# Optimization experiments

Measured on AMD Instinct MI355X. Metric: run time of the kernel, lower is better.

## Reference

```python
import jax, jax.numpy as jnp
import numpy as np

B = 16
H = 56
W = 56
C = 384
NH = 12
HD = C // NH
WS = 7
SHIFT = 3
N = WS * WS
SCALE = HD ** -0.5
EPS = 1e-3  # keras LayerNormalization default epsilon


def _rel_pos_index():
    coords = np.stack(np.meshgrid(np.arange(WS), np.arange(WS), indexing='ij')).reshape(2, -1)
    rel = (coords[:, :, None] - coords[:, None, :]).transpose(1, 2, 0)
    rel[:, :, 0] += WS - 1
    rel[:, :, 1] += WS - 1
    rel[:, :, 0] *= 2 * WS - 1
    return rel.sum(-1)  # [N, N]

REL_IDX = jnp.asarray(_rel_pos_index())


def _shift_mask():
    # faithful reproduction of the TransformerBlock.__init__ mask construction
    mask = np.zeros((1, H, W, 1), np.float32)
    slices = (slice(0, -WS), slice(-WS, -SHIFT), slice(-SHIFT, None))
    cnt = 0
    for hs in slices:
        for ws in slices:
            mask[:, hs, ws, :] = cnt
            cnt += 1
    mw = mask.reshape(1, H // WS, WS, W // WS, WS, 1).transpose(0, 1, 3, 2, 4, 5).reshape(-1, N)
    m = mw[:, None, :] - mw[:, :, None]  # expand_dims(mw,1) - expand_dims(mw,2)
    return np.where(m != 0, np.float32(-100.0), np.float32(0.0))  # [nw, N, N]

MASK = jnp.asarray(_shift_mask())


def _ln(x, g, b):
    mu = x.mean(-1, keepdims=True)
    var = ((x - mu) ** 2).mean(-1, keepdims=True)
    return (x - mu) / jnp.sqrt(var + EPS) * g + b


def _window_partition(x):  # [B,H,W,C] -> [B*nw, N, C]
    b = x.shape[0]
    x = x.reshape(b, H // WS, WS, W // WS, WS, C).transpose(0, 1, 3, 2, 4, 5)
    return x.reshape(-1, N, C)


def _window_reverse(wins, b):  # [B*nw, WS, WS, C] -> [B,H,W,C]
    x = wins.reshape(b, H // WS, W // WS, WS, WS, C).transpose(0, 1, 3, 2, 4, 5)
    return x.reshape(b, H, W, C)


def setup_inputs() -> dict:
    key = jax.random.key(0)
    ks = jax.random.split(key, 8)
    s = 0.02
    return {
        'x': jax.random.normal(ks[0], (B, H * W, C), jnp.float32),
        'ln1_g': jnp.ones((C,), jnp.float32),
        'ln1_b': jnp.zeros((C,), jnp.float32),
        'ln2_g': jnp.ones((C,), jnp.float32),
        'ln2_b': jnp.zeros((C,), jnp.float32),
        'qkv_w': s * jax.random.normal(ks[1], (C, 3 * C), jnp.float32),
        'qkv_b': jnp.zeros((3 * C,), jnp.float32),
        'proj_w': s * jax.random.normal(ks[2], (C, C), jnp.float32),
        'proj_b': jnp.zeros((C,), jnp.float32),
        'mlp_w1': s * jax.random.normal(ks[3], (C, 4 * C), jnp.float32),
        'mlp_b1': jnp.zeros((4 * C,), jnp.float32),
        'mlp_w2': s * jax.random.normal(ks[4], (4 * C, C), jnp.float32),
        'mlp_b2': jnp.zeros((C,), jnp.float32),
        'rel_pos_table': s * jax.random.normal(ks[5], ((2 * WS - 1) * (2 * WS - 1), NH), jnp.float32),
    }


def reference(x, ln1_g, ln1_b, ln2_g, ln2_b, qkv_w, qkv_b, proj_w, proj_b,
              mlp_w1, mlp_b1, mlp_w2, mlp_b2, rel_pos_table):
    skip = x
    y = _ln(x, ln1_g, ln1_b).reshape(B, H, W, C)
    # cyclic shift (faithful to source: shift=(-s, +s))
    y = jnp.roll(y, shift=(-SHIFT, SHIFT), axis=(1, 2))
    wins = _window_partition(y)                      # [nW, N, C]
    nW = wins.shape[0]

    qkv = wins @ qkv_w + qkv_b                       # [nW, N, 3C]
    qkv = qkv.reshape(nW, N, 3, NH, HD).transpose(2, 0, 3, 1, 4)
    q, k, v = qkv[0] * SCALE, qkv[1], qkv[2]         # [nW, NH, N, HD]

    attn = jnp.einsum('whnd,whmd->whnm', q, k)       # [nW, NH, N, N]
    bias = rel_pos_table[REL_IDX.reshape(-1)].reshape(N, N, NH).transpose(2, 0, 1)
    attn = attn + bias[None]

    nw = MASK.shape[0]
    attn = attn.reshape(nW // nw, nw, NH, N, N) + MASK[None, :, None]
    attn = jax.nn.softmax(attn.reshape(nW, NH, N, N), axis=-1)

    out = jnp.einsum('whnm,whmd->wnhd', attn, v).reshape(nW, N, C)
    out = out @ proj_w + proj_b

    y = _window_reverse(out.reshape(-1, WS, WS, C), B)
    # reverse shift (faithful to source: shift=(+s, +s))
    y = jnp.roll(y, shift=(SHIFT, SHIFT), axis=(1, 2))
    x = y.reshape(B, H * W, C) + skip

    skip = x
    y = _ln(x, ln2_g, ln2_b)
    y = jax.nn.gelu(y @ mlp_w1 + mlp_b1, approximate=False)
    y = y @ mlp_w2 + mlp_b2
    return y + skip
```

## Files before the change

### kernel.cpp

```cpp
#include <hip/hip_runtime.h>
#include <hip/hip_bf16.h>
#include <math.h>

typedef __hip_bfloat16 bf16;
typedef unsigned short ushort_t;
typedef __bf16 bf16x8 __attribute__((ext_vector_type(8)));
typedef float f32x4 __attribute__((ext_vector_type(4)));

#define TOKENS 50176
#define CW2 512
#define CROWS2 (CW2 * 49)
#define SCALE_ 0.17677669529663687f

__device__ __forceinline__ float b2f(bf16 v) { return __bfloat162float(v); }
__device__ __forceinline__ bf16  f2b(float v) { return __float2bfloat16(v); }

__device__ __forceinline__ float gelu_f(float v) {
  float x = v * 0.7071067811865475f;
  float ax = fabsf(x);
  float t = 1.f / (1.f + 0.3275911f * ax);
  float poly = ((((1.061405429f * t - 1.453152027f) * t + 1.421413741f) * t
                 - 0.284496736f) * t + 0.254829592f) * t;
  float erfv = 1.f - poly * __expf(-ax * ax);
  erfv = copysignf(erfv, x);
  return 0.5f * v * (1.f + erfv);
}

__global__ __launch_bounds__(256) void wt_bf16(const float* __restrict__ W,
                                               ushort_t* __restrict__ Wt,
                                               int K, int N) {
  int idx = blockIdx.x * 256 + threadIdx.x;
  if (idx >= K * N) return;
  int n = idx / K, k = idx - n * K;
  bf16 h = f2b(W[(size_t)k * N + n]);
  Wt[idx] = *(ushort_t*)&h;
}

__global__ __launch_bounds__(64) void ln1_kernel(const float* __restrict__ x,
                                                 const float* __restrict__ g,
                                                 const float* __restrict__ bta,
                                                 bf16* __restrict__ wins) {
  int t = blockIdx.x;
  int lane = threadIdx.x;
  int w = t / 49, n = t - w * 49;
  int bi = w >> 6, wi = w & 63;
  int hw = wi >> 3, ww = wi & 7;
  int ti = n / 7, tj = n - ti * 7;
  int hr = hw * 7 + ti, wr = ww * 7 + tj;
  int hs = (hr + 3) % 56;
  int wsc = (wr + 53) % 56;
  const float* row = x + ((size_t)bi * 3136 + hs * 56 + wsc) * 384;
  float v[6];
  float s = 0.f, s2 = 0.f;
#pragma unroll
  for (int j = 0; j < 6; ++j) {
    v[j] = row[lane + 64 * j];
    s += v[j]; s2 += v[j] * v[j];
  }
#pragma unroll
  for (int m = 32; m >= 1; m >>= 1) {
    s  += __shfl_xor(s, m, 64);
    s2 += __shfl_xor(s2, m, 64);
  }
  float mu = s * (1.f / 384.f);
  float var = s2 * (1.f / 384.f) - mu * mu;
  float rstd = rsqrtf(var + 1e-3f);
  bf16* orow = wins + (size_t)t * 384;
#pragma unroll
  for (int j = 0; j < 6; ++j) {
    int c = lane + 64 * j;
    orow[c] = f2b((v[j] - mu) * rstd * g[c] + bta[c]);
  }
}

__global__ __launch_bounds__(64) void ln2_kernel(const float* __restrict__ x1,
                                                 const float* __restrict__ g,
                                                 const float* __restrict__ bta,
                                                 bf16* __restrict__ out) {
  int t = blockIdx.x;
  int lane = threadIdx.x;
  const float* row = x1 + (size_t)t * 384;
  float v[6];
  float s = 0.f, s2 = 0.f;
#pragma unroll
  for (int j = 0; j < 6; ++j) {
    v[j] = row[lane + 64 * j];
    s += v[j]; s2 += v[j] * v[j];
  }
#pragma unroll
  for (int m = 32; m >= 1; m >>= 1) {
    s  += __shfl_xor(s, m, 64);
    s2 += __shfl_xor(s2, m, 64);
  }
  float mu = s * (1.f / 384.f);
  float var = s2 * (1.f / 384.f) - mu * mu;
  float rstd = rsqrtf(var + 1e-3f);
  bf16* orow = out + (size_t)t * 384;
#pragma unroll
  for (int j = 0; j < 6; ++j) {
    int c = lane + 64 * j;
    orow[c] = f2b((v[j] - mu) * rstd * g[c] + bta[c]);
  }
}

template<int MODE>
__global__ __launch_bounds__(512, 6) void mfma_gemm(
    const ushort_t* __restrict__ A, const ushort_t* __restrict__ Bt,
    const float* __restrict__ bias, int N, int K,
    const float* __restrict__ resid, void* __restrict__ out_) {
  __shared__ ushort_t As[128 * 32];
  __shared__ ushort_t Bs[128 * 32];
  int tid = threadIdx.x;
  int lane = tid & 63, wv = tid >> 6;
  int wm = wv >> 1, wn = wv & 1;
  int lm = lane & 15, kg = lane >> 4;

  int nwg = gridDim.x;
  int q = nwg >> 3, r = nwg & 7;
  int xcd = blockIdx.x & 7, ii = blockIdx.x >> 3;
  int l = ((xcd < r) ? xcd * (q + 1) : r * (q + 1) + (xcd - r) * q) + ii;
  int nxt = N >> 7;
  int col0 = (l % nxt) * 128, row0 = (l / nxt) * 128;

  f32x4 acc[2][4];
#pragma unroll
  for (int i = 0; i < 2; ++i)
#pragma unroll
    for (int j = 0; j < 4; ++j) acc[i][j] = (f32x4){0.f, 0.f, 0.f, 0.f};

  int rsub = lane >> 2;
  int bsrc = (lane & 3) ^ ((rsub >> 1) & 3);
  int pbr = kg ^ ((lm >> 1) & 3);

  const ushort_t* gA = &A[(size_t)(row0 + wv * 16 + rsub) * K + bsrc * 8];
  const ushort_t* gB = &Bt[(size_t)(col0 + wv * 16 + rsub) * K + bsrc * 8];

  int NT = K >> 5;
  for (int t = 0; t < NT; ++t) {
    __builtin_amdgcn_global_load_lds(
        (const __attribute__((address_space(1))) void*)(gA + (t << 5)),
        (__attribute__((address_space(3))) void*)&As[wv * 512], 16, 0, 0);
    __builtin_amdgcn_global_load_lds(
        (const __attribute__((address_space(1))) void*)(gB + (t << 5)),
        (__attribute__((address_space(3))) void*)&Bs[wv * 512], 16, 0, 0);
    __syncthreads();
    bf16x8 a[2], b[4];
#pragma unroll
    for (int i = 0; i < 2; ++i) {
      int ra = wm * 32 + i * 16 + lm;
      a[i] = *(const bf16x8*)&As[ra * 32 + pbr * 8];
    }
#pragma unroll
    for (int j = 0; j < 4; ++j) {
      int rb = wn * 64 + j * 16 + lm;
      b[j] = *(const bf16x8*)&Bs[rb * 32 + pbr * 8];
    }
#pragma unroll
    for (int i = 0; i < 2; ++i)
#pragma unroll
      for (int j = 0; j < 4; ++j)
        acc[i][j] = __builtin_amdgcn_mfma_f32_16x16x32_bf16(a[i], b[j], acc[i][j], 0, 0, 0);
    __syncthreads();
  }

  int m0 = row0 + wm * 32, n0 = col0 + wn * 64;
#pragma unroll
  for (int i = 0; i < 2; ++i) {
#pragma unroll
    for (int reg = 0; reg < 4; ++reg) {
      int m = m0 + i * 16 + kg * 4 + reg;
      size_t obase = 0;
      if (MODE == 1) {
        int w = m / 49, nn = m - w * 49;
        int bi = w >> 6, wi = w & 63;
        int hw = wi >> 3, ww = wi & 7;
        int ti = nn / 7, tj = nn - ti * 7;
        int hf = (hw * 7 + ti + 3) % 56, wf = (ww * 7 + tj + 3) % 56;
        obase = ((size_t)bi * 3136 + hf * 56 + wf) * 384;
      }
#pragma unroll
      for (int j = 0; j < 4; ++j) {
        int cN = n0 + j * 16 + lm;
        float v = acc[i][j][reg] + bias[cN];
        if (MODE == 0) {
          ((bf16*)out_)[(size_t)m * N + cN] = f2b(v);
        } else if (MODE == 1) {
          float* O = (float*)out_;
          O[obase + cN] = v + resid[obase + cN];
        } else if (MODE == 2) {
          ((bf16*)out_)[(size_t)m * N + cN] = f2b(gelu_f(v));
        } else {
          float* O = (float*)out_;
          O[(size_t)m * N + cN] = v + resid[(size_t)m * N + cN];
        }
      }
    }
  }
}

__global__ __launch_bounds__(256) void attn_mfma(const ushort_t* __restrict__ qkv_c,
                                                 const float* __restrict__ table,
                                                 ushort_t* __restrict__ attn_c,
                                                 int w_base) {
  int wl = blockIdx.x >> 2, hg = blockIdx.x & 3;
  int w = w_base + wl;
  int wi = w & 63;
  int hw = wi >> 3, ww = wi & 7;
  __shared__ ushort_t Qs[64 * 40];
  __shared__ ushort_t Ks[64 * 40];
  __shared__ ushort_t Vt[32 * 72];
  __shared__ ushort_t Ps[64 * 72];
  __shared__ float bias_s[169 * 12];
  int tid = threadIdx.x;
  int lane = tid & 63, wv = tid >> 6;
  int lm = lane & 15, kg = lane >> 4;

  for (int i = tid; i < 64 * 40; i += 256) { Qs[i] = 0; Ks[i] = 0; }
  for (int i = tid; i < 32 * 72; i += 256) Vt[i] = 0;
  for (int i = tid; i < 169 * 12; i += 256) bias_s[i] = table[i];
  __syncthreads();

  for (int hh = 0; hh < 3; ++hh) {
    int h = hg * 3 + hh;
    const ushort_t* base = qkv_c + (size_t)wl * 49 * 1152 + h * 32;
    for (int idx = tid; idx < 392; idx += 256) {
      int n = idx >> 3, d0 = (idx & 7) * 4;
      const ushort_t* p = base + (size_t)n * 1152 + d0;
      ushort4 q = *(const ushort4*)(p);
      ushort4 k = *(const ushort4*)(p + 384);
      ushort4 v = *(const ushort4*)(p + 768);
      *(ushort4*)&Qs[n * 40 + d0] = q;
      *(ushort4*)&Ks[n * 40 + d0] = k;
      Vt[(d0 + 0) * 72 + n] = v.x;
      Vt[(d0 + 1) * 72 + n] = v.y;
      Vt[(d0 + 2) * 72 + n] = v.z;
      Vt[(d0 + 3) * 72 + n] = v.w;
    }
    __syncthreads();

    bf16x8 qa = *(const bf16x8*)&Qs[(wv * 16 + lm) * 40 + kg * 8];
    f32x4 sacc[4];
#pragma unroll
    for (int jt = 0; jt < 4; ++jt) {
      bf16x8 kb = *(const bf16x8*)&Ks[(jt * 16 + lm) * 40 + kg * 8];
      sacc[jt] = __builtin_amdgcn_mfma_f32_16x16x32_bf16(
          qa, kb, (f32x4){0.f, 0.f, 0.f, 0.f}, 0, 0, 0);
    }

    int i_base = wv * 16 + kg * 4;
#pragma unroll
    for (int reg = 0; reg < 4; ++reg) {
      int i = i_base + reg;
      int ii = (i < 49) ? i : 0;
      int yi = ii / 7, xi = ii - yi * 7;
      int hri = hw * 7 + yi, wri = ww * 7 + xi;
      int ri = (hri < 49 ? 0 : (hri < 53 ? 1 : 2)) * 3 + (wri < 49 ? 0 : (wri < 53 ? 1 : 2));
      float sv[4];
      float mx = -1e30f;
#pragma unroll
      for (int jt = 0; jt < 4; ++jt) {
        int j = jt * 16 + lm;
        int jj = (j < 49) ? j : 0;
        int yj = jj / 7, xj = jj - yj * 7;
        int hrj = hw * 7 + yj, wrj = ww * 7 + xj;
        int rj = (hrj < 49 ? 0 : (hrj < 53 ? 1 : 2)) * 3 + (wrj < 49 ? 0 : (wrj < 53 ? 1 : 2));
        int ridx = (yi - yj + 6) * 13 + (xi - xj + 6);
        float s = sacc[jt][reg] * SCALE_ + bias_s[ridx * 12 + h] + ((ri == rj) ? 0.f : -100.f);
        sv[jt] = (j < 49) ? s : -1e30f;
        mx = fmaxf(mx, sv[jt]);
      }
#pragma unroll
      for (int msk = 1; msk < 16; msk <<= 1) mx = fmaxf(mx, __shfl_xor(mx, msk, 64));
      float sm = 0.f;
#pragma unroll
      for (int jt = 0; jt < 4; ++jt) {
        float e = ((jt * 16 + lm) < 49) ? __expf(sv[jt] - mx) : 0.f;
        sv[jt] = e; sm += e;
      }
#pragma unroll
      for (int msk = 1; msk < 16; msk <<= 1) sm += __shfl_xor(sm, msk, 64);
      float inv = 1.f / sm;
#pragma unroll
      for (int jt = 0; jt < 4; ++jt) {
        bf16 pb = f2b(sv[jt] * inv);
        Ps[(size_t)i * 72 + jt * 16 + lm] = *(ushort_t*)&pb;
      }
    }
    f32x4 oacc[2] = {(f32x4){0.f, 0.f, 0.f, 0.f}, (f32x4){0.f, 0.f, 0.f, 0.f}};
#pragma unroll
    for (int ks = 0; ks < 2; ++ks) {
      bf16x8 pa = *(const bf16x8*)&Ps[(wv * 16 + lm) * 72 + ks * 32 + kg * 8];
#pragma unroll
      for (int dt = 0; dt < 2; ++dt) {
        bf16x8 vb = *(const bf16x8*)&Vt[(dt * 16 + lm) * 72 + ks * 32 + kg * 8];
        oacc[dt] = __builtin_amdgcn_mfma_f32_16x16x32_bf16(pa, vb, oacc[dt], 0, 0, 0);
      }
    }
#pragma unroll
    for (int reg = 0; reg < 4; ++reg) {
      int r = i_base + reg;
      if (r < 49) {
#pragma unroll
        for (int dt = 0; dt < 2; ++dt) {
          bf16 ob = f2b(oacc[dt][reg]);
          attn_c[((size_t)wl * 49 + r) * 384 + h * 32 + dt * 16 + lm] = *(ushort_t*)&ob;
        }
      }
    }
    __syncthreads();
  }
}

extern "C" void kernel_launch(void* const* d_in, const int* in_sizes, int n_in,
                              void* d_out, int out_size, void* d_ws, size_t ws_size,
                              hipStream_t stream) {
  const float* x      = (const float*)d_in[0];
  const float* ln1_g  = (const float*)d_in[1];
  const float* ln1_b  = (const float*)d_in[2];
  const float* ln2_g  = (const float*)d_in[3];
  const float* ln2_b  = (const float*)d_in[4];
  const float* qkv_w  = (const float*)d_in[5];
  const float* qkv_b  = (const float*)d_in[6];
  const float* proj_w = (const float*)d_in[7];
  const float* proj_b = (const float*)d_in[8];
  const float* mlp_w1 = (const float*)d_in[9];
  const float* mlp_b1 = (const float*)d_in[10];
  const float* mlp_w2 = (const float*)d_in[11];
  const float* mlp_b2 = (const float*)d_in[12];
  const float* rel_tb = (const float*)d_in[13];

  char* ws = (char*)d_ws;
  ushort_t* r0 = (ushort_t*)(ws + 0);
  ushort_t* r1 = (ushort_t*)(ws + 38535168ull);
  ushort_t* wq = (ushort_t*)(ws + 115605504ull);
  ushort_t* wp = wq + 442368;
  ushort_t* w1 = wp + 147456;
  ushort_t* w2 = w1 + 589824;
  float* out = (float*)d_out;

  wt_bf16<<<1728, 256, 0, stream>>>(qkv_w, wq, 384, 1152);
  wt_bf16<<<576, 256, 0, stream>>>(proj_w, wp, 384, 384);
  wt_bf16<<<2304, 256, 0, stream>>>(mlp_w1, w1, 384, 1536);
  wt_bf16<<<2304, 256, 0, stream>>>(mlp_w2, w2, 1536, 384);

  ln1_kernel<<<TOKENS, 64, 0, stream>>>(x, ln1_g, ln1_b, (bf16*)r0);

  for (int c = 0; c < 2; ++c) {
    ushort_t* winc = r0 + (size_t)c * CROWS2 * 384;
    mfma_gemm<0><<<(CROWS2 / 128) * 9, 512, 0, stream>>>(
        winc, wq, qkv_b, 1152, 384, nullptr, (void*)r1);
    attn_mfma<<<CW2 * 4, 256, 0, stream>>>(r1, rel_tb, winc, c * CW2);
  }

  mfma_gemm<1><<<(TOKENS / 128) * 3, 512, 0, stream>>>(
      r0, wp, proj_b, 384, 384, x, (void*)out);

  ln2_kernel<<<TOKENS, 64, 0, stream>>>(out, ln2_g, ln2_b, (bf16*)r0);

  for (int c = 0; c < 2; ++c) {
    ushort_t* lc = r0 + (size_t)c * CROWS2 * 384;
    float* oc = out + (size_t)c * CROWS2 * 384;
    mfma_gemm<2><<<(CROWS2 / 128) * 12, 512, 0, stream>>>(
        lc, w1, mlp_b1, 1536, 384, nullptr, (void*)r1);
    mfma_gemm<3><<<(CROWS2 / 128) * 3, 512, 0, stream>>>(
        r1, w2, mlp_b2, 384, 1536, oc, (void*)oc);
  }
}
```

Before: 600.2 us.

## Enlarge GEMM row tile to 256 and merge weight-transpose launches

The GEMM kernel now computes two 128-row A sub-tiles per block against one shared B tile, so each block covers 256 rows and B-tile loads are reused across twice the rows. Accumulator count doubles and the occupancy hint drops from 6 to 4 blocks per CU, which raises register use and lowers the number of resident blocks. The four weight-transpose launches are merged into a single kernel that dispatches on the global index to cut launch overhead. Row counts (25088 and 50176) divide evenly by 256, so grid sizes stay exact.

```diff
diff --git a/kernel.cpp b/kernel.cpp
--- a/kernel.cpp
+++ b/kernel.cpp
@@ -26,14 +26,24 @@
   return 0.5f * v * (1.f + erfv);
 }
 
-__global__ __launch_bounds__(256) void wt_bf16(const float* __restrict__ W,
-                                               ushort_t* __restrict__ Wt,
-                                               int K, int N) {
+__global__ __launch_bounds__(256) void wt_all(const float* __restrict__ qkv_w,
+                                              const float* __restrict__ proj_w,
+                                              const float* __restrict__ mlp_w1,
+                                              const float* __restrict__ mlp_w2,
+                                              ushort_t* __restrict__ wq,
+                                              ushort_t* __restrict__ wp,
+                                              ushort_t* __restrict__ w1,
+                                              ushort_t* __restrict__ w2) {
   int idx = blockIdx.x * 256 + threadIdx.x;
-  if (idx >= K * N) return;
-  int n = idx / K, k = idx - n * K;
+  const float* W; ushort_t* O; int K, N, loc;
+  if (idx < 442368)        { W = qkv_w;  O = wq; K = 384;  N = 1152; loc = idx; }
+  else if (idx < 589824)   { W = proj_w; O = wp; K = 384;  N = 384;  loc = idx - 442368; }
+  else if (idx < 1179648)  { W = mlp_w1; O = w1; K = 384;  N = 1536; loc = idx - 589824; }
+  else if (idx < 1769472)  { W = mlp_w2; O = w2; K = 1536; N = 384;  loc = idx - 1179648; }
+  else return;
+  int n = loc / K, k = loc - n * K;
   bf16 h = f2b(W[(size_t)k * N + n]);
-  Wt[idx] = *(ushort_t*)&h;
+  O[loc] = *(ushort_t*)&h;
 }
 
 __global__ __launch_bounds__(64) void ln1_kernel(const float* __restrict__ x,
@@ -104,11 +114,11 @@
 }
 
 template<int MODE>
-__global__ __launch_bounds__(512, 6) void mfma_gemm(
+__global__ __launch_bounds__(512, 4) void mfma_gemm(
     const ushort_t* __restrict__ A, const ushort_t* __restrict__ Bt,
     const float* __restrict__ bias, int N, int K,
     const float* __restrict__ resid, void* __restrict__ out_) {
-  __shared__ ushort_t As[128 * 32];
+  __shared__ ushort_t As[2][128 * 32];
   __shared__ ushort_t Bs[128 * 32];
   int tid = threadIdx.x;
   int lane = tid & 63, wv = tid >> 6;
@@ -120,78 +130,92 @@
   int xcd = blockIdx.x & 7, ii = blockIdx.x >> 3;
   int l = ((xcd < r) ? xcd * (q + 1) : r * (q + 1) + (xcd - r) * q) + ii;
   int nxt = N >> 7;
-  int col0 = (l % nxt) * 128, row0 = (l / nxt) * 128;
-
-  f32x4 acc[2][4];
-#pragma unroll
-  for (int i = 0; i < 2; ++i)
-#pragma unroll
-    for (int j = 0; j < 4; ++j) acc[i][j] = (f32x4){0.f, 0.f, 0.f, 0.f};
+  int col0 = (l % nxt) * 128, row0 = (l / nxt) * 256;
+
+  f32x4 acc[2][2][4];
+#pragma unroll
+  for (int rt = 0; rt < 2; ++rt)
+#pragma unroll
+    for (int i = 0; i < 2; ++i)
+#pragma unroll
+      for (int j = 0; j < 4; ++j) acc[rt][i][j] = (f32x4){0.f, 0.f, 0.f, 0.f};
 
   int rsub = lane >> 2;
   int bsrc = (lane & 3) ^ ((rsub >> 1) & 3);
   int pbr = kg ^ ((lm >> 1) & 3);
 
-  const ushort_t* gA = &A[(size_t)(row0 + wv * 16 + rsub) * K + bsrc * 8];
-  const ushort_t* gB = &Bt[(size_t)(col0 + wv * 16 + rsub) * K + bsrc * 8];
+  const ushort_t* gA0 = &A[(size_t)(row0 + wv * 16 + rsub) * K + bsrc * 8];
+  const ushort_t* gA1 = gA0 + (size_t)128 * K;
+  const ushort_t* gB  = &Bt[(size_t)(col0 + wv * 16 + rsub) * K + bsrc * 8];
 
   int NT = K >> 5;
   for (int t = 0; t < NT; ++t) {
     __builtin_amdgcn_global_load_lds(
-        (const __attribute__((address_space(1))) void*)(gA + (t << 5)),
-        (__attribute__((address_space(3))) void*)&As[wv * 512], 16, 0, 0);
+        (const __attribute__((address_space(1))) void*)(gA0 + (t << 5)),
+        (__attribute__((address_space(3))) void*)&As[0][wv * 512], 16, 0, 0);
+    __builtin_amdgcn_global_load_lds(
+        (const __attribute__((address_space(1))) void*)(gA1 + (t << 5)),
+        (__attribute__((address_space(3))) void*)&As[1][wv * 512], 16, 0, 0);
     __builtin_amdgcn_global_load_lds(
         (const __attribute__((address_space(1))) void*)(gB + (t << 5)),
         (__attribute__((address_space(3))) void*)&Bs[wv * 512], 16, 0, 0);
     __syncthreads();
-    bf16x8 a[2], b[4];
-#pragma unroll
-    for (int i = 0; i < 2; ++i) {
-      int ra = wm * 32 + i * 16 + lm;
-      a[i] = *(const bf16x8*)&As[ra * 32 + pbr * 8];
-    }
+    bf16x8 b[4];
 #pragma unroll
     for (int j = 0; j < 4; ++j) {
       int rb = wn * 64 + j * 16 + lm;
       b[j] = *(const bf16x8*)&Bs[rb * 32 + pbr * 8];
     }
 #pragma unroll
-    for (int i = 0; i < 2; ++i)
-#pragma unroll
-      for (int j = 0; j < 4; ++j)
-        acc[i][j] = __builtin_amdgcn_mfma_f32_16x16x32_bf16(a[i], b[j], acc[i][j], 0, 0, 0);
+    for (int rt = 0; rt < 2; ++rt) {
+      bf16x8 a[2];
+#pragma unroll
+      for (int i = 0; i < 2; ++i) {
+        int ra = wm * 32 + i * 16 + lm;
+        a[i] = *(const bf16x8*)&As[rt][ra * 32 + pbr * 8];
+      }
+#pragma unroll
+      for (int i = 0; i < 2; ++i)
+#pragma unroll
+        for (int j = 0; j < 4; ++j)
+          acc[rt][i][j] = __builtin_amdgcn_mfma_f32_16x16x32_bf16(a[i], b[j], acc[rt][i][j], 0, 0, 0);
+    }
     __syncthreads();
   }
 
-  int m0 = row0 + wm * 32, n0 = col0 + wn * 64;
-#pragma unroll
-  for (int i = 0; i < 2; ++i) {
-#pragma unroll
-    for (int reg = 0; reg < 4; ++reg) {
-      int m = m0 + i * 16 + kg * 4 + reg;
-      size_t obase = 0;
-      if (MODE == 1) {
-        int w = m / 49, nn = m - w * 49;
-        int bi = w >> 6, wi = w & 63;
-        int hw = wi >> 3, ww = wi & 7;
-        int ti = nn / 7, tj = nn - ti * 7;
-        int hf = (hw * 7 + ti + 3) % 56, wf = (ww * 7 + tj + 3) % 56;
-        obase = ((size_t)bi * 3136 + hf * 56 + wf) * 384;
-      }
-#pragma unroll
-      for (int j = 0; j < 4; ++j) {
-        int cN = n0 + j * 16 + lm;
-        float v = acc[i][j][reg] + bias[cN];
-        if (MODE == 0) {
-          ((bf16*)out_)[(size_t)m * N + cN] = f2b(v);
-        } else if (MODE == 1) {
-          float* O = (float*)out_;
-          O[obase + cN] = v + resid[obase + cN];
-        } else if (MODE == 2) {
-          ((bf16*)out_)[(size_t)m * N + cN] = f2b(gelu_f(v));
-        } else {
-          float* O = (float*)out_;
-          O[(size_t)m * N + cN] = v + resid[(size_t)m * N + cN];
+  int n0 = col0 + wn * 64;
+#pragma unroll
+  for (int rt = 0; rt < 2; ++rt) {
+    int m0 = row0 + rt * 128 + wm * 32;
+#pragma unroll
+    for (int i = 0; i < 2; ++i) {
+#pragma unroll
+      for (int reg = 0; reg < 4; ++reg) {
+        int m = m0 + i * 16 + kg * 4 + reg;
+        size_t obase = 0;
+        if (MODE == 1) {
+          int w = m / 49, nn = m - w * 49;
+          int bi = w >> 6, wi = w & 63;
+          int hw = wi >> 3, ww = wi & 7;
+          int ti = nn / 7, tj = nn - ti * 7;
+          int hf = (hw * 7 + ti + 3) % 56, wf = (ww * 7 + tj + 3) % 56;
+          obase = ((size_t)bi * 3136 + hf * 56 + wf) * 384;
+        }
+#pragma unroll
+        for (int j = 0; j < 4; ++j) {
+          int cN = n0 + j * 16 + lm;
+          float v = acc[rt][i][j][reg] + bias[cN];
+          if (MODE == 0) {
+            ((bf16*)out_)[(size_t)m * N + cN] = f2b(v);
+          } else if (MODE == 1) {
+            float* O = (float*)out_;
+            O[obase + cN] = v + resid[obase + cN];
+          } else if (MODE == 2) {
+            ((bf16*)out_)[(size_t)m * N + cN] = f2b(gelu_f(v));
+          } else {
+            float* O = (float*)out_;
+            O[(size_t)m * N + cN] = v + resid[(size_t)m * N + cN];
+          }
         }
       }
     }
@@ -338,21 +362,18 @@
   ushort_t* w2 = w1 + 589824;
   float* out = (float*)d_out;
 
-  wt_bf16<<<1728, 256, 0, stream>>>(qkv_w, wq, 384, 1152);
-  wt_bf16<<<576, 256, 0, stream>>>(proj_w, wp, 384, 384);
-  wt_bf16<<<2304, 256, 0, stream>>>(mlp_w1, w1, 384, 1536);
-  wt_bf16<<<2304, 256, 0, stream>>>(mlp_w2, w2, 1536, 384);
+  wt_all<<<6912, 256, 0, stream>>>(qkv_w, proj_w, mlp_w1, mlp_w2, wq, wp, w1, w2);
 
   ln1_kernel<<<TOKENS, 64, 0, stream>>>(x, ln1_g, ln1_b, (bf16*)r0);
 
   for (int c = 0; c < 2; ++c) {
     ushort_t* winc = r0 + (size_t)c * CROWS2 * 384;
-    mfma_gemm<0><<<(CROWS2 / 128) * 9, 512, 0, stream>>>(
+    mfma_gemm<0><<<(CROWS2 / 256) * 9, 512, 0, stream>>>(
         winc, wq, qkv_b, 1152, 384, nullptr, (void*)r1);
     attn_mfma<<<CW2 * 4, 256, 0, stream>>>(r1, rel_tb, winc, c * CW2);
   }
 
-  mfma_gemm<1><<<(TOKENS / 128) * 3, 512, 0, stream>>>(
+  mfma_gemm<1><<<(TOKENS / 256) * 3, 512, 0, stream>>>(
       r0, wp, proj_b, 384, 384, x, (void*)out);
 
   ln2_kernel<<<TOKENS, 64, 0, stream>>>(out, ln2_g, ln2_b, (bf16*)r0);
@@ -360,9 +381,9 @@
   for (int c = 0; c < 2; ++c) {
     ushort_t* lc = r0 + (size_t)c * CROWS2 * 384;
     float* oc = out + (size_t)c * CROWS2 * 384;
-    mfma_gemm<2><<<(CROWS2 / 128) * 12, 512, 0, stream>>>(
+    mfma_gemm<2><<<(CROWS2 / 256) * 12, 512, 0, stream>>>(
         lc, w1, mlp_b1, 1536, 384, nullptr, (void*)r1);
-    mfma_gemm<3><<<(CROWS2 / 128) * 3, 512, 0, stream>>>(
+    mfma_gemm<3><<<(CROWS2 / 256) * 3, 512, 0, stream>>>(
         r1, w2, mlp_b2, 384, 1536, oc, (void*)oc);
   }
 }
```

Measured after the change: 617.4 us. 1.03x slower.
